# Kernel tuning notes

Hardware: AMD Instinct MI355X
Metric: run time of the kernel (lower is better)

## Reference

```python
import jax, jax.numpy as jnp
import numpy as np
from jax import lax

EPS = 1e-5
K = 3  # DCN kernel size


def _conv(x, w, pad, lhs_dil=(1, 1)):
    return lax.conv_general_dilated(
        x, w, window_strides=(1, 1), padding=((pad, pad), (pad, pad)),
        lhs_dilation=lhs_dil, dimension_numbers=('NCHW', 'OIHW', 'NCHW'))


def _batchnorm(x, gamma, beta):
    # training-mode BN (batch statistics), matching nn.BatchNorm2d in train()
    m = jnp.mean(x, axis=(0, 2, 3), keepdims=True)
    v = jnp.var(x, axis=(0, 2, 3), keepdims=True)
    return (x - m) * lax.rsqrt(v + EPS) * gamma[None, :, None, None] + beta[None, :, None, None]


def _bilinear_sample(x, py, px):
    # x: [B,C,H,W]; py,px: [B,K2,H,W] fractional sample coords (zero-pad outside)
    B, C, H, W = x.shape
    K2 = py.shape[1]
    y0 = jnp.floor(py)
    x0 = jnp.floor(px)
    wy = (py - y0)[:, None]  # [B,1,K2,H,W]
    wx = (px - x0)[:, None]
    xf = x.reshape(B, C, H * W)

    def gather(yi, xi):
        valid = ((yi >= 0) & (yi <= H - 1) & (xi >= 0) & (xi <= W - 1)).astype(x.dtype)
        yc = jnp.clip(yi, 0, H - 1).astype(jnp.int32)
        xc = jnp.clip(xi, 0, W - 1).astype(jnp.int32)
        idx = (yc * W + xc).reshape(B, 1, -1)
        v = jnp.take_along_axis(xf, idx, axis=2).reshape(B, C, K2, H, W)
        return v * valid[:, None]

    v00 = gather(y0, x0)
    v01 = gather(y0, x0 + 1)
    v10 = gather(y0 + 1, x0)
    v11 = gather(y0 + 1, x0 + 1)
    return (v00 * (1 - wy) * (1 - wx) + v01 * (1 - wy) * wx
            + v10 * wy * (1 - wx) + v11 * wy * wx)  # [B,C,K2,H,W]


def _dcn(x, w_off, b_off, w_dcn, b_dcn):
    # Modulated deformable conv (DCNv2), stride 1, pad 1, dil 1, 1 deform group
    B, C, H, W = x.shape
    K2 = K * K
    om = _conv(x, w_off, pad=1) + b_off[None, :, None, None]  # [B,3*K2,H,W]
    dy, dx, m = om[:, :K2], om[:, K2:2 * K2], jax.nn.sigmoid(om[:, 2 * K2:])
    ki, kj = jnp.meshgrid(jnp.arange(K), jnp.arange(K), indexing='ij')
    ky = (ki.reshape(-1) - 1).astype(x.dtype)[None, :, None, None]
    kx = (kj.reshape(-1) - 1).astype(x.dtype)[None, :, None, None]
    py = dy + jnp.arange(H, dtype=x.dtype)[None, None, :, None] + ky
    px = dx + jnp.arange(W, dtype=x.dtype)[None, None, None, :] + kx
    val = _bilinear_sample(x, py, px) * m[:, None]  # [B,C,K2,H,W]
    Co = w_dcn.shape[0]
    out = jnp.einsum('bikhw,oik->bohw', val, w_dcn.reshape(Co, C, K2))
    return out + b_dcn[None, :, None, None]


def _conv_transpose(x, w_up):
    # torch ConvTranspose2d(k=4, stride=2, pad=1), weight [Cin, Cout, 4, 4]
    w = jnp.flip(w_up, axis=(2, 3)).transpose(1, 0, 2, 3)  # -> OIHW
    return _conv(x, w, pad=2, lhs_dil=(2, 2))


def setup_inputs() -> dict:
    key = jax.random.key(0)
    ks = jax.random.split(key, 8)
    B, Cin, Cout, H, W = 4, 256, 256, 64, 64
    x = jax.random.normal(ks[0], (B, Cin, H, W), dtype=jnp.float32)
    w_off = jax.random.normal(ks[1], (3 * K * K, Cin, K, K), dtype=jnp.float32) * 0.01
    b_off = jnp.zeros((3 * K * K,), dtype=jnp.float32)
    w_dcn = jax.random.normal(ks[2], (Cout, Cin, K, K), dtype=jnp.float32) * (1.0 / np.sqrt(Cin * K * K))
    b_dcn = jnp.zeros((Cout,), dtype=jnp.float32)
    gamma1 = jax.random.uniform(ks[3], (Cout,), dtype=jnp.float32, minval=0.5, maxval=1.5)
    beta1 = jax.random.normal(ks[4], (Cout,), dtype=jnp.float32) * 0.1
    w_up = jax.random.normal(ks[5], (Cout, Cout, 4, 4), dtype=jnp.float32) * (1.0 / np.sqrt(Cout * 16))
    gamma2 = jax.random.uniform(ks[6], (Cout,), dtype=jnp.float32, minval=0.5, maxval=1.5)
    beta2 = jax.random.normal(ks[7], (Cout,), dtype=jnp.float32) * 0.1
    return {'x': x, 'w_off': w_off, 'b_off': b_off, 'w_dcn': w_dcn, 'b_dcn': b_dcn,
            'gamma1': gamma1, 'beta1': beta1, 'w_up': w_up, 'gamma2': gamma2, 'beta2': beta2}


def reference(x, w_off, b_off, w_dcn, b_dcn, gamma1, beta1, w_up, gamma2, beta2):
    out = _dcn(x, w_off, b_off, w_dcn, b_dcn)
    out = jax.nn.relu(_batchnorm(out, gamma1, beta1))
    out = _conv_transpose(out, w_up)
    out = jax.nn.relu(_batchnorm(out, gamma2, beta2))
    return out
```

## Files before the change

kernel.cpp:

```cpp
#include <hip/hip_runtime.h>
#include <hip/hip_bf16.h>
#include <math.h>

#define B_   4
#define CIN  256
#define COUT 256
#define HW   4096

typedef __attribute__((ext_vector_type(8))) short short8;
typedef __attribute__((ext_vector_type(4))) float float4v;

#define LSTR  40
#define LSTR2 72
#define LSTR4 136

__device__ __forceinline__ float sigmoidf_(float v){ return 1.0f/(1.0f+expf(-v)); }
__device__ __forceinline__ ushort f2bf(float f){
  union { float f; unsigned u; } x; x.f = f;
  unsigned r = x.u + 0x7fffu + ((x.u>>16)&1u);
  return (ushort)(r>>16);
}
__device__ __forceinline__ float bflo(unsigned u){ union{unsigned u; float f;} c; c.u = u<<16;          return c.f; }
__device__ __forceinline__ float bfhi(unsigned u){ union{unsigned u; float f;} c; c.u = u & 0xffff0000u; return c.f; }

__global__ void k_transpose_x(const float* __restrict__ x, ushort* __restrict__ xtb){
  __shared__ float ts[32][33];
  int tx = threadIdx.x & 31, ty = threadIdx.x >> 5;
  int p0 = blockIdx.x * 32, c0 = blockIdx.y * 32, b = blockIdx.z;
  const float* xb = x + (size_t)b*CIN*HW;
#pragma unroll
  for(int q=0;q<4;q++){
    int c = ty + q*8;
    ts[c][tx] = xb[(size_t)(c0+c)*HW + p0+tx];
  }
  __syncthreads();
#pragma unroll
  for(int q=0;q<4;q++){
    int pr = ty + q*8;
    xtb[((size_t)(b*HW + p0+pr)<<8) + c0+tx] = f2bf(ts[tx][pr]);
  }
}

__global__ void k_build_all(const float* __restrict__ w_off, const float* __restrict__ w_dcn,
                            const float* __restrict__ w_up,
                            ushort* __restrict__ Wob, ushort* __restrict__ Wdb,
                            ushort* __restrict__ WT2c){
  int bid = blockIdx.x;
  if(bid < 288){
    int f = bid*256 + threadIdx.x;
    int kc = f>>10, o = (f>>5)&31, kk = f&31;
    int k = kc*32 + kk, tap = k>>8, c = k&255;
    float v = (o < 27) ? w_off[(size_t)o*2304 + c*9 + tap] : 0.f;
    Wob[f] = f2bf(v);
  } else if(bid < 288+2304){
    int f = (bid-288)*256 + threadIdx.x;
    int kc = f>>13, o = (f>>5)&255, kk = f&31;
    int k = kc>>3, c = ((kc&7)<<5) | kk;
    Wdb[f] = f2bf(w_dcn[(size_t)o*2304 + c*9 + k]);
  } else {
    int f = (bid-2592)*256 + threadIdx.x;
    int pp = f>>18, kc = (f>>13)&31, o = (f>>5)&255, kk = f&31;
    int k = kc*32 + kk, ab = k>>8, c = k&255;
    int a = ab>>1, bb = ab&1, ph = pp>>1, pw = pp&1;
    WT2c[f] = f2bf(w_up[(size_t)(c*COUT+o)*16 + (3-ph-2*a)*4 + (3-pw-2*bb)]);
  }
}

__global__ __launch_bounds__(256) void k_offset_mfma(const ushort* __restrict__ xtb,
                        const ushort* __restrict__ Wob, float* __restrict__ om2){
  __shared__ ushort Vs[2][64*LSTR4];
  __shared__ int sIdx[576];
  int tid = threadIdx.x;
  int fb  = blockIdx.x + (blockIdx.y<<6);
  int b   = (fb&7)>>1;
  int px0 = ((((fb>>3)<<1) | (fb&1))) << 6;
  int z   = blockIdx.z;
  for(int t=tid; t<576; t+=256){
    int tap = t>>6, px = t&63;
    int p = px0+px, hh = p>>6, ww = p&63;
    int ih = hh + tap/3 - 1, iw = ww + tap%3 - 1;
    sIdx[t] = (ih>=0 && ih<64 && iw>=0 && iw<64) ? ((b*HW + ih*64+iw)<<8) : -1;
  }
  __syncthreads();

  int lane = tid&63, wv = tid>>6, lo = lane&15, hi = lane>>4;
  float4v acc[2];
  acc[0] = acc[1] = (float4v){0.f,0.f,0.f,0.f};
  int vpx = tid>>2, vseg = tid&3;
  const int wlane = lo*32 + hi*8;

#define OFF_WLOAD_ALLQ(Q, W) do{ \
    _Pragma("unroll") \
    for(int c_=0;c_<4;c_++){ \
      const ushort* wp_ = Wob + (((Q)*4+c_)<<10) + wlane; \
      W[2*c_+0] = *(const short8*)(wp_); \
      W[2*c_+1] = *(const short8*)(wp_ + 512); \
    } \
  }while(0)

#define OFF_GATHER_Q(Q, V) do{ \
    int k_ = (Q)>>1, c0_ = ((Q)&1)<<7; \
    int idx_ = sIdx[(k_<<6)+vpx]; \
    int coff_ = c0_ + (vseg<<5); \
    V[0]=make_uint4(0,0,0,0); V[1]=make_uint4(0,0,0,0); \
    V[2]=make_uint4(0,0,0,0); V[3]=make_uint4(0,0,0,0); \
    if(idx_ >= 0){ \
      V[0] = *(const uint4*)(xtb + idx_ + coff_); \
      V[1] = *(const uint4*)(xtb + idx_ + coff_ + 8); \
      V[2] = *(const uint4*)(xtb + idx_ + coff_ + 16); \
      V[3] = *(const uint4*)(xtb + idx_ + coff_ + 24); \
    } \
  }while(0)

#define OFF_VWRITE_Q(V, BUF) do{ \
    ushort* vp_ = &Vs[BUF][vpx*LSTR4 + (vseg<<5)]; \
    *(uint4*)(vp_)      = V[0]; \
    *(uint4*)(vp_ + 8)  = V[1]; \
    *(uint4*)(vp_ + 16) = V[2]; \
    *(uint4*)(vp_ + 24) = V[3]; \
  }while(0)

#define OFF_COMPUTE_Q2(W, BUF) do{ \
    const ushort* bp_ = &Vs[BUF][(wv*16+lo)*LSTR4 + hi*8]; \
    _Pragma("unroll") \
    for(int c_=0;c_<4;c_++){ \
      short8 ba_ = *(const short8*)(bp_ + c_*32); \
      acc[0] = __builtin_amdgcn_mfma_f32_16x16x32_bf16(W[2*c_+0], ba_, acc[0], 0,0,0); \
      acc[1] = __builtin_amdgcn_mfma_f32_16x16x32_bf16(W[2*c_+1], ba_, acc[1], 0,0,0); \
    } \
  }while(0)

  short8 w[8];
  uint4 vE[4];
  OFF_GATHER_Q(z*9, vE);
  OFF_VWRITE_Q(vE, 0);
  __syncthreads();

#pragma unroll 1
  for(int pc=0; pc<9; ++pc){
    int cur = pc&1;
    int q = z*9 + pc;
    OFF_WLOAD_ALLQ(q, w);
    if(pc<8) OFF_GATHER_Q(q+1, vE);
    OFF_COMPUTE_Q2(w, cur);
    if(pc<8) OFF_VWRITE_Q(vE, cur^1);
    __syncthreads();
  }
  int p = px0 + wv*16 + lo;
#pragma unroll
  for(int mi=0;mi<2;mi++){
    int ob = mi*16 + hi*4;
    float4v a = (mi==0) ? acc[0] : acc[1];
#pragma unroll
    for(int r=0;r<4;r++){
      int o = ob + r;
      if(o < 27) om2[(size_t)((z*B_+b)*27+o)*HW + p] = a[r];
    }
  }
}

#define DCN_WLOAD_ALLQ(Q, W) do{ \
    _Pragma("unroll") \
    for(int c_=0;c_<4;c_++){ \
      const ushort* wp_ = Wdb + ((size_t)((Q)*4+c_)<<13) + wlane; \
      W[4*c_+0] = *(const short8*)(wp_); \
      W[4*c_+1] = *(const short8*)(wp_ + 512); \
      W[4*c_+2] = *(const short8*)(wp_ + 1024); \
      W[4*c_+3] = *(const short8*)(wp_ + 1536); \
    } \
  }while(0)

#define DCN_GATHER_Q(Q, C, CF) do{ \
    int k_ = (Q)>>1, c0_ = ((Q)&1)<<7; \
    int t_ = (k_<<6) + vpx; \
    int pk_ = sPk[t_]; CF = sCf[t_]; \
    int coff_ = c0_ + (vseg<<4); \
    int iy0_=pk_&63, iy1_=(pk_>>6)&63, ix0_=(pk_>>12)&63, ix1_=(pk_>>18)&63; \
    const ushort* p00_ = xtb + cbase + (((iy0_<<6)+ix0_)<<8) + coff_; \
    const ushort* p01_ = xtb + cbase + (((iy0_<<6)+ix1_)<<8) + coff_; \
    const ushort* p10_ = xtb + cbase + (((iy1_<<6)+ix0_)<<8) + coff_; \
    const ushort* p11_ = xtb + cbase + (((iy1_<<6)+ix1_)<<8) + coff_; \
    C[0] = *(const uint4*)(p00_);     C[4] = *(const uint4*)(p00_ + 8); \
    C[1] = *(const uint4*)(p01_);     C[5] = *(const uint4*)(p01_ + 8); \
    C[2] = *(const uint4*)(p10_);     C[6] = *(const uint4*)(p10_ + 8); \
    C[3] = *(const uint4*)(p11_);     C[7] = *(const uint4*)(p11_ + 8); \
  }while(0)

#define DCN_BLEND_H(C0,C1,C2,C3, CF, DST) do{ \
    union{ ushort us[8]; uint4 q; } rr_; \
    rr_.us[0] = f2bf(CF.x*bflo(C0.x)+CF.y*bflo(C1.x)+CF.z*bflo(C2.x)+CF.w*bflo(C3.x)); \
    rr_.us[1] = f2bf(CF.x*bfhi(C0.x)+CF.y*bfhi(C1.x)+CF.z*bfhi(C2.x)+CF.w*bfhi(C3.x)); \
    rr_.us[2] = f2bf(CF.x*bflo(C0.y)+CF.y*bflo(C1.y)+CF.z*bflo(C2.y)+CF.w*bflo(C3.y)); \
    rr_.us[3] = f2bf(CF.x*bfhi(C0.y)+CF.y*bfhi(C1.y)+CF.z*bfhi(C2.y)+CF.w*bfhi(C3.y)); \
    rr_.us[4] = f2bf(CF.x*bflo(C0.z)+CF.y*bflo(C1.z)+CF.z*bflo(C2.z)+CF.w*bflo(C3.z)); \
    rr_.us[5] = f2bf(CF.x*bfhi(C0.z)+CF.y*bfhi(C1.z)+CF.z*bfhi(C2.z)+CF.w*bfhi(C3.z)); \
    rr_.us[6] = f2bf(CF.x*bflo(C0.w)+CF.y*bflo(C1.w)+CF.z*bflo(C2.w)+CF.w*bflo(C3.w)); \
    rr_.us[7] = f2bf(CF.x*bfhi(C0.w)+CF.y*bfhi(C1.w)+CF.z*bfhi(C2.w)+CF.w*bfhi(C3.w)); \
    *(uint4*)(DST) = rr_.q; \
  }while(0)

#define DCN_BLEND_Q(C, CF, BUF) do{ \
    ushort* dp_ = &Vs[BUF][vpx*LSTR4 + (vseg<<4)]; \
    DCN_BLEND_H(C[0],C[1],C[2],C[3], CF, dp_); \
    DCN_BLEND_H(C[4],C[5],C[6],C[7], CF, dp_ + 8); \
  }while(0)

#define DCN_COMPUTE_Q2(W, BUF) do{ \
    const ushort* bp_ = &Vs[BUF][(pn0+lo)*LSTR4 + hi*8]; \
    _Pragma("unroll") \
    for(int c_=0;c_<4;c_++){ \
      short8 b0_ = *(const short8*)(bp_ + c_*32); \
      short8 b1_ = *(const short8*)(bp_ + c_*32 + 16*LSTR4); \
      acc[0][0] = __builtin_amdgcn_mfma_f32_16x16x32_bf16(W[4*c_+0], b0_, acc[0][0], 0,0,0); \
      acc[0][1] = __builtin_amdgcn_mfma_f32_16x16x32_bf16(W[4*c_+0], b1_, acc[0][1], 0,0,0); \
      acc[1][0] = __builtin_amdgcn_mfma_f32_16x16x32_bf16(W[4*c_+1], b0_, acc[1][0], 0,0,0); \
      acc[1][1] = __builtin_amdgcn_mfma_f32_16x16x32_bf16(W[4*c_+1], b1_, acc[1][1], 0,0,0); \
      acc[2][0] = __builtin_amdgcn_mfma_f32_16x16x32_bf16(W[4*c_+2], b0_, acc[2][0], 0,0,0); \
      acc[2][1] = __builtin_amdgcn_mfma_f32_16x16x32_bf16(W[4*c_+2], b1_, acc[2][1], 0,0,0); \
      acc[3][0] = __builtin_amdgcn_mfma_f32_16x16x32_bf16(W[4*c_+3], b0_, acc[3][0], 0,0,0); \
      acc[3][1] = __builtin_amdgcn_mfma_f32_16x16x32_bf16(W[4*c_+3], b1_, acc[3][1], 0,0,0); \
    } \
  }while(0)

__global__ __launch_bounds__(512) void k_dcn_mfma(const ushort* __restrict__ xtb,
                        const float* __restrict__ om2, const float* __restrict__ b_off,
                        const ushort* __restrict__ Wdb, ushort* __restrict__ out1u){
  __shared__ ushort Vs[2][64*LSTR4];
  __shared__ int    sPk[576];
  __shared__ float4 sCf[576];
  int tid = threadIdx.x;
  int fb  = blockIdx.x + (blockIdx.y<<6);
  int b   = (fb&7)>>1;
  int px0 = ((((fb>>3)<<1) | (fb&1))) << 6;

  for(int t=tid; t<576; t+=512){
    int k = t>>6, px = t&63;
    int p = px0 + px, hh = p>>6, ww = p&63;
    const float* oma = om2 + (size_t)b*27*HW + p;
    const float* omb = oma + (size_t)B_*27*HW;
    float dy = oma[(size_t)k*HW]      + omb[(size_t)k*HW]      + b_off[k];
    float dx = oma[(size_t)(9+k)*HW]  + omb[(size_t)(9+k)*HW]  + b_off[9+k];
    float mo = sigmoidf_(oma[(size_t)(18+k)*HW] + omb[(size_t)(18+k)*HW] + b_off[18+k]);
    float py  = dy + (float)(hh + k/3 - 1);
    float pxf = dx + (float)(ww + k%3 - 1);
    float y0 = floorf(py), x0 = floorf(pxf);
    float wy = py - y0, wx = pxf - x0;
    float y1 = y0 + 1.0f, x1 = x0 + 1.0f;
    bool vy0 = (y0>=0.f)&&(y0<=63.f), vy1 = (y1>=0.f)&&(y1<=63.f);
    bool vx0 = (x0>=0.f)&&(x0<=63.f), vx1 = (x1>=0.f)&&(x1<=63.f);
    int iy0 = (int)fminf(fmaxf(y0,0.f),63.f);
    int iy1 = (int)fminf(fmaxf(y1,0.f),63.f);
    int ix0 = (int)fminf(fmaxf(x0,0.f),63.f);
    int ix1 = (int)fminf(fmaxf(x1,0.f),63.f);
    sPk[t] = iy0 | (iy1<<6) | (ix0<<12) | (ix1<<18);
    sCf[t] = make_float4((vy0&&vx0)? (1.f-wy)*(1.f-wx)*mo : 0.f,
                         (vy0&&vx1)? (1.f-wy)*wx*mo       : 0.f,
                         (vy1&&vx0)? wy*(1.f-wx)*mo       : 0.f,
                         (vy1&&vx1)? wy*wx*mo             : 0.f);
  }
  __syncthreads();

  int lane = tid&63, wv = tid>>6, lo = lane&15, hi = lane>>4;
  int om0 = (wv>>1)*64, pn0 = (wv&1)*32;
  float4v acc[4][2];
#pragma unroll
  for(int i=0;i<4;i++)
#pragma unroll
    for(int j=0;j<2;j++) acc[i][j] = (float4v){0.f,0.f,0.f,0.f};
  int cbase = (b*HW)<<8;
  int vpx = tid>>3, vseg = tid&7;
  const int wlane = (om0+lo)*32 + hi*8;

  short8 w[16];
  uint4 cE[8];
  float4 fE;

  DCN_GATHER_Q(0, cE, fE);
  DCN_BLEND_Q(cE, fE, 0);
  __syncthreads();

#pragma unroll 1
  for(int pc=0; pc<18; ++pc){
    int cur = pc&1;
    DCN_WLOAD_ALLQ(pc, w);
    if(pc<17) DCN_GATHER_Q(pc+1, cE, fE);
    DCN_COMPUTE_Q2(w, cur);
    if(pc<17) DCN_BLEND_Q(cE, fE, cur^1);
    __syncthreads();
  }

  ushort* op0 = out1u + ((size_t)(b*COUT)<<12) + px0 + pn0 + lo;
#pragma unroll
  for(int i=0;i<4;i++){
    int ob = om0 + i*16 + hi*4;
#pragma unroll
    for(int r=0;r<4;r++){
      int o = ob + r;
      ushort* op = op0 + ((size_t)o<<12);
      op[0]  = f2bf(acc[i][0][r]);
      op[16] = f2bf(acc[i][1][r]);
    }
  }
}

__global__ void k_bn_stats_bf1(const ushort* __restrict__ out1u, float* __restrict__ stats){
  int o = blockIdx.x, tid = threadIdx.x;
  float s=0.f, ss=0.f;
  for(int b=0;b<B_;b++){
    const ushort* p = out1u + ((size_t)(b*COUT+o)<<12);
    for(int i=tid*8; i<4096; i+=2048){
      uint4 v = *(const uint4*)(p + i);
      float f;
      f=bflo(v.x); s+=f; ss+=f*f;  f=bfhi(v.x); s+=f; ss+=f*f;
      f=bflo(v.y); s+=f; ss+=f*f;  f=bfhi(v.y); s+=f; ss+=f*f;
      f=bflo(v.z); s+=f; ss+=f*f;  f=bfhi(v.z); s+=f; ss+=f*f;
      f=bflo(v.w); s+=f; ss+=f*f;  f=bfhi(v.w); s+=f; ss+=f*f;
    }
  }
  __shared__ float rs[256], rss[256];
  rs[tid]=s; rss[tid]=ss; __syncthreads();
  for(int st=128; st>0; st>>=1){
    if(tid<st){ rs[tid]+=rs[tid+st]; rss[tid]+=rss[tid+st]; }
    __syncthreads();
  }
  if(tid==0){
    float n = (float)(B_*HW);
    float mean = rs[0]/n;
    float var  = rss[0]/n - mean*mean;
    stats[o*2] = mean; stats[o*2+1] = rsqrtf(var + 1e-5f);
  }
}

__global__ void k_bn_stats_ct(const ushort* __restrict__ ct, float* __restrict__ stats){
  int o = blockIdx.x, tid = threadIdx.x;
  float s=0.f, ss=0.f;
  for(int pl=0; pl<16; ++pl){
    const ushort* p = ct + (((size_t)(pl*256 + o))<<12);
    for(int i=tid*8; i<4096; i+=2048){
      uint4 v = *(const uint4*)(p + i);
      float f;
      f=bflo(v.x); s+=f; ss+=f*f;  f=bfhi(v.x); s+=f; ss+=f*f;
      f=bflo(v.y); s+=f; ss+=f*f;  f=bfhi(v.y); s+=f; ss+=f*f;
      f=bflo(v.z); s+=f; ss+=f*f;  f=bfhi(v.z); s+=f; ss+=f*f;
      f=bflo(v.w); s+=f; ss+=f*f;  f=bfhi(v.w); s+=f; ss+=f*f;
    }
  }
  __shared__ float rs[256], rss[256];
  rs[tid]=s; rss[tid]=ss; __syncthreads();
  for(int st=128; st>0; st>>=1){
    if(tid<st){ rs[tid]+=rs[tid+st]; rss[tid]+=rss[tid+st]; }
    __syncthreads();
  }
  if(tid==0){
    float n = (float)(16*4096);
    float mean = rs[0]/n;
    float var  = rss[0]/n - mean*mean;
    stats[o*2] = mean; stats[o*2+1] = rsqrtf(var + 1e-5f);
  }
}

__global__ void k_bn1_apply_t(const ushort* __restrict__ out1u, const float* __restrict__ stats,
                              const float* __restrict__ gamma, const float* __restrict__ beta,
                              ushort* __restrict__ y1b){
  __shared__ float ts[32][33];
  int tx = threadIdx.x & 31, ty = threadIdx.x >> 5;
  int p0 = blockIdx.x*32, o0 = blockIdx.y*32, b = blockIdx.z;
#pragma unroll
  for(int q=0;q<4;q++){
    int oo = ty + q*8; int o = o0 + oo;
    float m = stats[o*2], rstd = stats[o*2+1];
    float scale = rstd * gamma[o];
    float shift = beta[o] - m * scale;
    float v = bflo((unsigned)out1u[((size_t)(b*COUT+o)<<12) + p0+tx]);
    ts[oo][tx] = fmaxf(v*scale + shift, 0.f);
  }
  __syncthreads();
#pragma unroll
  for(int q=0;q<4;q++){
    int pr = ty + q*8;
    y1b[((size_t)(b*HW + p0+pr)<<8) + o0+tx] = f2bf(ts[tx][pr]);
  }
}

__global__ __launch_bounds__(512) void k_convt_mfma(const ushort* __restrict__ y1b,
                        const ushort* __restrict__ WT2c,
                        ushort* __restrict__ ct){
  __shared__ ushort Vs[2][256*LSTR2];
  __shared__ int sIdx[1024];
  int tid = threadIdx.x;
  int fb  = blockIdx.x + (blockIdx.y<<4) + (blockIdx.z<<6);
  int jj = fb&7, rr2 = fb>>3;
  int b   = jj>>1;
  int pp  = ((rr2>>4)<<1) | (jj&1);
  int px0 = (rr2&15) << 8;
  int ph = pp>>1, pw = pp&1;

  for(int t=tid; t<1024; t+=512){
    int ab = t>>8, px = t&255;
    int a = ab>>1, bb = ab&1;
    int p = px0+px, r = p>>6, s = p&63;
    int ih = r + ph - 1 + a, iw = s + pw - 1 + bb;
    sIdx[t] = (ih>=0 && ih<64 && iw>=0 && iw<64) ? ((b*HW + ih*64+iw)<<8) : -1;
  }
  __syncthreads();

  int lane = tid&63, wv = tid>>6, lo = lane&15, hi = lane>>4;
  int om0 = (wv>>1)*64;
  int pn0 = (wv&1)*128;
  float4v acc[4][8];
#pragma unroll
  for(int i=0;i<4;i++)
#pragma unroll
    for(int j=0;j<8;j++) acc[i][j] = (float4v){0.f,0.f,0.f,0.f};

  const ushort* wbase = WT2c + ((size_t)pp<<18);
  const int wlaneb = (om0+lo)*32 + hi*8;
  int vpx = tid>>1, vseg = tid&1;
  uint4 vpre[4];

#define CT3_PREFETCH(PC) do{ \
    int kc0_ = (PC)*2; \
    int ab_ = kc0_>>3, c0_ = (kc0_&7)<<5; \
    int idx_ = sIdx[(ab_<<8) + vpx]; \
    int co_ = c0_ + vseg*32; \
    vpre[0]=make_uint4(0,0,0,0); vpre[1]=make_uint4(0,0,0,0); \
    vpre[2]=make_uint4(0,0,0,0); vpre[3]=make_uint4(0,0,0,0); \
    if(idx_ >= 0){ \
      vpre[0] = *(const uint4*)(y1b + idx_ + co_); \
      vpre[1] = *(const uint4*)(y1b + idx_ + co_ + 8); \
      vpre[2] = *(const uint4*)(y1b + idx_ + co_ + 16); \
      vpre[3] = *(const uint4*)(y1b + idx_ + co_ + 24); \
    } \
  }while(0)

#define CT3_WRITE(BUF) do{ \
    ushort* vp_ = &Vs[BUF][vpx*LSTR2 + vseg*32]; \
    *(uint4*)(vp_)      = vpre[0]; \
    *(uint4*)(vp_ + 8)  = vpre[1]; \
    *(uint4*)(vp_ + 16) = vpre[2]; \
    *(uint4*)(vp_ + 24) = vpre[3]; \
  }while(0)

  CT3_PREFETCH(0);
  CT3_WRITE(0);
  __syncthreads();

#pragma unroll 1
  for(int pc=0; pc<16; ++pc){
    int cur = pc&1;
    if(pc < 15) CT3_PREFETCH(pc+1);
#pragma unroll
    for(int c=0; c<2; ++c){
      const ushort* wp = wbase + ((size_t)(((pc<<1)|c))<<13) + wlaneb;
      const ushort* bp = &Vs[cur][(pn0+lo)*LSTR2 + c*32 + hi*8];
      short8 bfr[8];
#pragma unroll
      for(int j=0;j<8;j++) bfr[j] = *(const short8*)(bp + j*16*LSTR2);
#pragma unroll
      for(int i=0;i<4;i++){
        short8 afr = *(const short8*)(wp + i*512);
#pragma unroll
        for(int j=0;j<8;j++)
          acc[i][j] = __builtin_amdgcn_mfma_f32_16x16x32_bf16(afr, bfr[j], acc[i][j], 0,0,0);
      }
    }
    if(pc < 15) CT3_WRITE(cur^1);
    __syncthreads();
  }

  ushort* cb = ct + (((size_t)(pp*4 + b)*256)<<12);
#pragma unroll
  for(int i=0;i<4;i++){
#pragma unroll
    for(int r=0;r<4;r++){
      int o = om0 + i*16 + hi*4 + r;
      ushort* row = cb + ((size_t)o<<12) + px0 + pn0 + lo;
#pragma unroll
      for(int j=0;j<8;j++) row[j*16] = f2bf(acc[i][j][r]);
    }
  }
}

__global__ void k_bn2_apply(const ushort* __restrict__ ct, const float* __restrict__ stats,
                            const float* __restrict__ gamma, const float* __restrict__ beta,
                            float* __restrict__ out){
  int gid = blockIdx.x*256 + threadIdx.x;
  int e4 = gid<<2;
  int b = e4>>22, o = (e4>>14)&255, q = e4&16383;
  int H2 = q>>7, W2 = q&127;
  int r = H2>>1, ph = H2&1, s0 = W2>>1;
  size_t base0 = (((size_t)((ph*2)*4 + b)*256 + o)<<12) + r*64 + s0;
  unsigned u0 = *(const unsigned*)(ct + base0);
  unsigned u1 = *(const unsigned*)(ct + base0 + ((size_t)4<<20));
  float m = stats[o*2], rstd = stats[o*2+1];
  float sc = rstd * gamma[o];
  float sh = beta[o] - m * sc;
  float4 v;
  v.x = fmaxf(bflo(u0)*sc + sh, 0.f);
  v.y = fmaxf(bflo(u1)*sc + sh, 0.f);
  v.z = fmaxf(bfhi(u0)*sc + sh, 0.f);
  v.w = fmaxf(bfhi(u1)*sc + sh, 0.f);
  *(float4*)(out + e4) = v;
}

extern "C" void kernel_launch(void* const* d_in, const int* in_sizes, int n_in,
                              void* d_out, int out_size, void* d_ws, size_t ws_size,
                              hipStream_t stream){
  (void)in_sizes; (void)n_in; (void)out_size; (void)ws_size;
  const float* x     = (const float*)d_in[0];
  const float* w_off = (const float*)d_in[1];
  const float* b_off = (const float*)d_in[2];
  const float* w_dcn = (const float*)d_in[3];
  const float* gamma1= (const float*)d_in[5];
  const float* beta1 = (const float*)d_in[6];
  const float* w_up  = (const float*)d_in[7];
  const float* gamma2= (const float*)d_in[8];
  const float* beta2 = (const float*)d_in[9];
  float* out = (float*)d_out;

  float* ws    = (float*)d_ws;
  ushort* ct   = (ushort*)ws;
  float* om2   = ws;
  ushort* xtb  = (ushort*)(ws + 884736);
  ushort* out1u= (ushort*)(ws + 884736 + 2097152);
  float* base2 = ws + 8388608;
  ushort* y1b  = (ushort*)base2;
  ushort* WT2c = (ushort*)(base2 + 2097152);
  ushort* Wdb  = (ushort*)(base2 + 2097152 + 524288);
  ushort* Wob  = (ushort*)(base2 + 2097152 + 524288 + 294912);
  float* st1   = base2 + 2097152 + 524288 + 294912 + 36864;
  float* st2   = st1 + 512;

  k_transpose_x <<<dim3(128,8,4), 256, 0, stream>>>(x, xtb);
  k_build_all   <<<6688, 256, 0, stream>>>(w_off, w_dcn, w_up, Wob, Wdb, WT2c);
  k_offset_mfma <<<dim3(64,4,2), 256, 0, stream>>>(xtb, Wob, om2);
  k_dcn_mfma    <<<dim3(64,4),   512, 0, stream>>>(xtb, om2, b_off, Wdb, out1u);
  k_bn_stats_bf1<<<256,  256, 0, stream>>>(out1u, st1);
  k_bn1_apply_t <<<dim3(128,8,4), 256, 0, stream>>>(out1u, st1, gamma1, beta1, y1b);
  k_convt_mfma  <<<dim3(16,4,4),  512, 0, stream>>>(y1b, WT2c, ct);
  k_bn_stats_ct <<<256,  256, 0, stream>>>(ct, st2);
  k_bn2_apply   <<<16384,256, 0, stream>>>(ct, st2, gamma2, beta2, out);
}
```

Measured before the change: 254.6 us.

## Shrink DCN K-chunk to 64 and double-buffer weights and gathers two stages ahead

The deformable-conv MFMA loop now works on 64-channel chunks (36 iterations) instead of 128-channel chunks (18), with a smaller LDS tile. Weights are double-buffered in registers, loaded one step ahead, and the bilinear gathers are prefetched two steps ahead, so global-load latency can overlap the MFMA work. The aim is lower register pressure and more latency hiding, at the cost of twice as many barriers and shorter MFMA bursts per iteration.

Result: no change. 255.0 us (+0.2%).

```diff
diff --git a/kernel.cpp b/kernel.cpp
--- a/kernel.cpp
+++ b/kernel.cpp
@@ -159,73 +159,58 @@
   }
 }
 
-#define DCN_WLOAD_ALLQ(Q, W) do{ \
-    _Pragma("unroll") \
-    for(int c_=0;c_<4;c_++){ \
-      const ushort* wp_ = Wdb + ((size_t)((Q)*4+c_)<<13) + wlane; \
-      W[4*c_+0] = *(const short8*)(wp_); \
-      W[4*c_+1] = *(const short8*)(wp_ + 512); \
-      W[4*c_+2] = *(const short8*)(wp_ + 1024); \
-      W[4*c_+3] = *(const short8*)(wp_ + 1536); \
-    } \
-  }while(0)
-
-#define DCN_GATHER_Q(Q, C, CF) do{ \
-    int k_ = (Q)>>1, c0_ = ((Q)&1)<<7; \
+#define DCN_GATHER_P(PAIR, C, CF) do{ \
+    int k_ = (PAIR)>>2, c0_ = ((PAIR)&3)<<6; \
     int t_ = (k_<<6) + vpx; \
     int pk_ = sPk[t_]; CF = sCf[t_]; \
-    int coff_ = c0_ + (vseg<<4); \
+    int coff_ = c0_ + (vseg<<3); \
     int iy0_=pk_&63, iy1_=(pk_>>6)&63, ix0_=(pk_>>12)&63, ix1_=(pk_>>18)&63; \
-    const ushort* p00_ = xtb + cbase + (((iy0_<<6)+ix0_)<<8) + coff_; \
-    const ushort* p01_ = xtb + cbase + (((iy0_<<6)+ix1_)<<8) + coff_; \
-    const ushort* p10_ = xtb + cbase + (((iy1_<<6)+ix0_)<<8) + coff_; \
-    const ushort* p11_ = xtb + cbase + (((iy1_<<6)+ix1_)<<8) + coff_; \
-    C[0] = *(const uint4*)(p00_);     C[4] = *(const uint4*)(p00_ + 8); \
-    C[1] = *(const uint4*)(p01_);     C[5] = *(const uint4*)(p01_ + 8); \
-    C[2] = *(const uint4*)(p10_);     C[6] = *(const uint4*)(p10_ + 8); \
-    C[3] = *(const uint4*)(p11_);     C[7] = *(const uint4*)(p11_ + 8); \
-  }while(0)
-
-#define DCN_BLEND_H(C0,C1,C2,C3, CF, DST) do{ \
+    C[0] = *(const uint4*)(xtb + cbase + (((iy0_<<6)+ix0_)<<8) + coff_); \
+    C[1] = *(const uint4*)(xtb + cbase + (((iy0_<<6)+ix1_)<<8) + coff_); \
+    C[2] = *(const uint4*)(xtb + cbase + (((iy1_<<6)+ix0_)<<8) + coff_); \
+    C[3] = *(const uint4*)(xtb + cbase + (((iy1_<<6)+ix1_)<<8) + coff_); \
+  }while(0)
+
+#define DCN_BLEND_P(C, CF, BUF) do{ \
     union{ ushort us[8]; uint4 q; } rr_; \
-    rr_.us[0] = f2bf(CF.x*bflo(C0.x)+CF.y*bflo(C1.x)+CF.z*bflo(C2.x)+CF.w*bflo(C3.x)); \
-    rr_.us[1] = f2bf(CF.x*bfhi(C0.x)+CF.y*bfhi(C1.x)+CF.z*bfhi(C2.x)+CF.w*bfhi(C3.x)); \
-    rr_.us[2] = f2bf(CF.x*bflo(C0.y)+CF.y*bflo(C1.y)+CF.z*bflo(C2.y)+CF.w*bflo(C3.y)); \
-    rr_.us[3] = f2bf(CF.x*bfhi(C0.y)+CF.y*bfhi(C1.y)+CF.z*bfhi(C2.y)+CF.w*bfhi(C3.y)); \
-    rr_.us[4] = f2bf(CF.x*bflo(C0.z)+CF.y*bflo(C1.z)+CF.z*bflo(C2.z)+CF.w*bflo(C3.z)); \
-    rr_.us[5] = f2bf(CF.x*bfhi(C0.z)+CF.y*bfhi(C1.z)+CF.z*bfhi(C2.z)+CF.w*bfhi(C3.z)); \
-    rr_.us[6] = f2bf(CF.x*bflo(C0.w)+CF.y*bflo(C1.w)+CF.z*bflo(C2.w)+CF.w*bflo(C3.w)); \
-    rr_.us[7] = f2bf(CF.x*bfhi(C0.w)+CF.y*bfhi(C1.w)+CF.z*bfhi(C2.w)+CF.w*bfhi(C3.w)); \
-    *(uint4*)(DST) = rr_.q; \
-  }while(0)
-
-#define DCN_BLEND_Q(C, CF, BUF) do{ \
-    ushort* dp_ = &Vs[BUF][vpx*LSTR4 + (vseg<<4)]; \
-    DCN_BLEND_H(C[0],C[1],C[2],C[3], CF, dp_); \
-    DCN_BLEND_H(C[4],C[5],C[6],C[7], CF, dp_ + 8); \
-  }while(0)
-
-#define DCN_COMPUTE_Q2(W, BUF) do{ \
-    const ushort* bp_ = &Vs[BUF][(pn0+lo)*LSTR4 + hi*8]; \
+    rr_.us[0] = f2bf(CF.x*bflo(C[0].x)+CF.y*bflo(C[1].x)+CF.z*bflo(C[2].x)+CF.w*bflo(C[3].x)); \
+    rr_.us[1] = f2bf(CF.x*bfhi(C[0].x)+CF.y*bfhi(C[1].x)+CF.z*bfhi(C[2].x)+CF.w*bfhi(C[3].x)); \
+    rr_.us[2] = f2bf(CF.x*bflo(C[0].y)+CF.y*bflo(C[1].y)+CF.z*bflo(C[2].y)+CF.w*bflo(C[3].y)); \
+    rr_.us[3] = f2bf(CF.x*bfhi(C[0].y)+CF.y*bfhi(C[1].y)+CF.z*bfhi(C[2].y)+CF.w*bfhi(C[3].y)); \
+    rr_.us[4] = f2bf(CF.x*bflo(C[0].z)+CF.y*bflo(C[1].z)+CF.z*bflo(C[2].z)+CF.w*bflo(C[3].z)); \
+    rr_.us[5] = f2bf(CF.x*bfhi(C[0].z)+CF.y*bfhi(C[1].z)+CF.z*bfhi(C[2].z)+CF.w*bfhi(C[3].z)); \
+    rr_.us[6] = f2bf(CF.x*bflo(C[0].w)+CF.y*bflo(C[1].w)+CF.z*bflo(C[2].w)+CF.w*bflo(C[3].w)); \
+    rr_.us[7] = f2bf(CF.x*bfhi(C[0].w)+CF.y*bfhi(C[1].w)+CF.z*bfhi(C[2].w)+CF.w*bfhi(C[3].w)); \
+    *(uint4*)(&Vs[BUF][vpx*LSTR2 + (vseg<<3)]) = rr_.q; \
+  }while(0)
+
+#define DCN_WLOAD_P(PAIR, W) do{ \
+    const ushort* wp_ = Wdb + ((size_t)((PAIR)*2)<<13) + wlane; \
+    W[0] = *(const short8*)(wp_);         W[1] = *(const short8*)(wp_ + 512); \
+    W[2] = *(const short8*)(wp_ + 1024);  W[3] = *(const short8*)(wp_ + 1536); \
+    W[4] = *(const short8*)(wp_ + 8192);  W[5] = *(const short8*)(wp_ + 8704); \
+    W[6] = *(const short8*)(wp_ + 9216);  W[7] = *(const short8*)(wp_ + 9728); \
+  }while(0)
+
+#define DCN_COMPUTE_P(W, BUF) do{ \
+    const ushort* bp_ = &Vs[BUF][(pn0+lo)*LSTR2 + hi*8]; \
+    short8 a0_ = *(const short8*)(bp_); \
+    short8 a1_ = *(const short8*)(bp_ + 16*LSTR2); \
+    short8 b0_ = *(const short8*)(bp_ + 32); \
+    short8 b1_ = *(const short8*)(bp_ + 32 + 16*LSTR2); \
     _Pragma("unroll") \
-    for(int c_=0;c_<4;c_++){ \
-      short8 b0_ = *(const short8*)(bp_ + c_*32); \
-      short8 b1_ = *(const short8*)(bp_ + c_*32 + 16*LSTR4); \
-      acc[0][0] = __builtin_amdgcn_mfma_f32_16x16x32_bf16(W[4*c_+0], b0_, acc[0][0], 0,0,0); \
-      acc[0][1] = __builtin_amdgcn_mfma_f32_16x16x32_bf16(W[4*c_+0], b1_, acc[0][1], 0,0,0); \
-      acc[1][0] = __builtin_amdgcn_mfma_f32_16x16x32_bf16(W[4*c_+1], b0_, acc[1][0], 0,0,0); \
-      acc[1][1] = __builtin_amdgcn_mfma_f32_16x16x32_bf16(W[4*c_+1], b1_, acc[1][1], 0,0,0); \
-      acc[2][0] = __builtin_amdgcn_mfma_f32_16x16x32_bf16(W[4*c_+2], b0_, acc[2][0], 0,0,0); \
-      acc[2][1] = __builtin_amdgcn_mfma_f32_16x16x32_bf16(W[4*c_+2], b1_, acc[2][1], 0,0,0); \
-      acc[3][0] = __builtin_amdgcn_mfma_f32_16x16x32_bf16(W[4*c_+3], b0_, acc[3][0], 0,0,0); \
-      acc[3][1] = __builtin_amdgcn_mfma_f32_16x16x32_bf16(W[4*c_+3], b1_, acc[3][1], 0,0,0); \
+    for(int i_=0;i_<4;i_++){ \
+      acc[i_][0] = __builtin_amdgcn_mfma_f32_16x16x32_bf16(W[i_],   a0_, acc[i_][0], 0,0,0); \
+      acc[i_][1] = __builtin_amdgcn_mfma_f32_16x16x32_bf16(W[i_],   a1_, acc[i_][1], 0,0,0); \
+      acc[i_][0] = __builtin_amdgcn_mfma_f32_16x16x32_bf16(W[4+i_], b0_, acc[i_][0], 0,0,0); \
+      acc[i_][1] = __builtin_amdgcn_mfma_f32_16x16x32_bf16(W[4+i_], b1_, acc[i_][1], 0,0,0); \
     } \
   }while(0)
 
 __global__ __launch_bounds__(512) void k_dcn_mfma(const ushort* __restrict__ xtb,
                         const float* __restrict__ om2, const float* __restrict__ b_off,
                         const ushort* __restrict__ Wdb, ushort* __restrict__ out1u){
-  __shared__ ushort Vs[2][64*LSTR4];
+  __shared__ ushort Vs[2][64*LSTR2];
   __shared__ int    sPk[576];
   __shared__ float4 sCf[576];
   int tid = threadIdx.x;
@@ -271,22 +256,32 @@
   int vpx = tid>>3, vseg = tid&7;
   const int wlane = (om0+lo)*32 + hi*8;
 
-  short8 w[16];
-  uint4 cE[8];
-  float4 fE;
-
-  DCN_GATHER_Q(0, cE, fE);
-  DCN_BLEND_Q(cE, fE, 0);
+  short8 wA[8], wB[8];
+  uint4 cE[4], cO[4];
+  float4 fE, fO;
+
+  DCN_WLOAD_P(0, wA);
+  DCN_GATHER_P(0, cE, fE);
+  DCN_BLEND_P(cE, fE, 0);
+  DCN_GATHER_P(1, cO, fO);
   __syncthreads();
 
 #pragma unroll 1
-  for(int pc=0; pc<18; ++pc){
-    int cur = pc&1;
-    DCN_WLOAD_ALLQ(pc, w);
-    if(pc<17) DCN_GATHER_Q(pc+1, cE, fE);
-    DCN_COMPUTE_Q2(w, cur);
-    if(pc<17) DCN_BLEND_Q(cE, fE, cur^1);
-    __syncthreads();
+  for(int pb=0; pb<36; pb+=2){
+    {
+      if(pb<34) DCN_GATHER_P(pb+2, cE, fE);
+      DCN_WLOAD_P(pb+1, wB);
+      DCN_COMPUTE_P(wA, 0);
+      DCN_BLEND_P(cO, fO, 1);
+      __syncthreads();
+    }
+    {
+      if(pb<33) DCN_GATHER_P(pb+3, cO, fO);
+      if(pb<34) DCN_WLOAD_P(pb+2, wA);
+      DCN_COMPUTE_P(wB, 1);
+      if(pb<34) DCN_BLEND_P(cE, fE, 0);
+      __syncthreads();
+    }
   }
 
   ushort* op0 = out1u + ((size_t)(b*COUT)<<12) + px0 + pn0 + lo;
```
